# Kernel tuning notes

Measured on AMD Instinct MI355X. Metric: run time of the kernel, lower is better.

Reference implementation:

```python
import jax, jax.numpy as jnp
import numpy as np

N_ELEC = 62      # electrodes per graph (fixed by RGNN/SEED)
BATCH = 4096     # number of graphs
IN_CH = 5
HID = 32
N_CLS = 3
K = 2            # SGConv propagation steps (num_layers)


def setup_inputs() -> dict:
    key = jax.random.key(0)
    k1, k2, k3, k4 = jax.random.split(key, 4)
    n_tril = N_ELEC * (N_ELEC + 1) // 2  # 1953 learned lower-tri weights
    x = jax.random.normal(k1, (BATCH * N_ELEC, IN_CH), jnp.float32)
    adj_tril = jax.random.uniform(k2, (n_tril,), jnp.float32)
    lin_w = jax.random.normal(k3, (HID, IN_CH), jnp.float32) * 0.3
    lin_b = jnp.zeros((HID,), jnp.float32)
    fc_w = jax.random.normal(k4, (N_CLS, HID), jnp.float32) * 0.2
    fc_b = jnp.zeros((N_CLS,), jnp.float32)
    # Dense per-graph edge list matching adj.reshape(-1).repeat(B):
    # edge e = b*3844 + i*62 + j has source row=b*62+i, target col=b*62+j.
    i = np.arange(N_ELEC, dtype=np.int32)
    src = np.repeat(i, N_ELEC)              # [3844]
    dst = np.tile(i, N_ELEC)                # [3844]
    off = (np.arange(BATCH, dtype=np.int32) * N_ELEC)[:, None]
    row = (src[None, :] + off).reshape(-1)  # [B*3844]
    col = (dst[None, :] + off).reshape(-1)
    edge_index = jnp.asarray(np.stack([row, col]))  # int32 [2, E]
    batch_idx = jnp.asarray(np.repeat(np.arange(BATCH, dtype=np.int32), N_ELEC))
    return dict(x=x, adj_tril=adj_tril, lin_w=lin_w, lin_b=lin_b,
                fc_w=fc_w, fc_b=fc_b, edge_index=edge_index, batch_idx=batch_idx)


def reference(x, adj_tril, lin_w, lin_b, fc_w, fc_b, edge_index, batch_idx):
    # Rebuild symmetric dense adjacency from learned lower-triangular params.
    xs, ys = np.tril_indices(N_ELEC)  # static indices
    A = jnp.zeros((N_ELEC, N_ELEC), x.dtype).at[xs, ys].set(adj_tril)
    A = A + A.T - jnp.diag(jnp.diag(A))
    w = jnp.tile(A.reshape(-1), BATCH)        # edge weights [E]
    row, col = edge_index[0], edge_index[1]
    n_nodes = BATCH * N_ELEC
    # Symmetric GCN norm: D^-1/2 A D^-1/2 over the edge list (self-loops
    # already present in the dense graph, so add_remaining_self_loops is a
    # pure edge reorder here).
    deg = jax.ops.segment_sum(jnp.abs(w), row, num_segments=n_nodes)
    safe_deg = jnp.where(deg > 0, deg, 1.0)
    dinv = jnp.where(deg > 0, jax.lax.rsqrt(safe_deg), 0.0)
    norm = dinv[row] * w * dinv[col]          # [E]
    # K rounds of gather-scale-scatter propagation (SGConv).
    h = x
    for _ in range(K):
        h = jax.ops.segment_sum(norm[:, None] * h[row], col, num_segments=n_nodes)
    h = jax.nn.relu(h @ lin_w.T + lin_b)       # SGConv linear + relu
    pooled = jax.ops.segment_sum(h, batch_idx, num_segments=BATCH)  # global_add_pool
    # dropout is identity in eval mode
    return pooled @ fc_w.T + fc_b              # [B, num_classes]
```

## Files before the change

### kernel.cpp

```cpp
#include <hip/hip_runtime.h>

#define NE 62
#define IC 5
#define NTRIL 1953
#define SA 68
#define MTOT 3844

__global__ __launch_bounds__(256) void build_M(const float* __restrict__ adj_tril,
                                               float* __restrict__ Mg) {
    __shared__ float A[NE * SA];
    __shared__ float dinv[NE];
    int tid = threadIdx.x;
    for (int t = tid; t < NTRIL; t += 256) {
        float v = adj_tril[t];
        float r = sqrtf((float)(8 * t + 1));
        int i = (int)((r - 1.0f) * 0.5f);
        while ((i + 1) * (i + 2) / 2 <= t) ++i;
        while (i * (i + 1) / 2 > t) --i;
        int j = t - i * (i + 1) / 2;
        A[i * SA + j] = v;
        A[j * SA + i] = v;
    }
    __syncthreads();
    if (tid < NE) {
        float s = 0.f;
        for (int k = 0; k < NE; ++k) s += fabsf(A[tid * SA + k]);
        dinv[tid] = (s > 0.f) ? rsqrtf(s) : 0.f;
    }
    __syncthreads();
    for (int g = tid; g < NE * NE; g += 256) {
        int i = g / NE, j = g % NE;
        A[i * SA + j] *= dinv[i] * dinv[j];
    }
    __syncthreads();
    int g = blockIdx.x * 256 + tid;
    if (g < NE * NE) {
        int r = g / NE, cidx = g % NE;
        const float4* ra = (const float4*)(A + r * SA);
        const float4* rb = (const float4*)(A + cidx * SA);
        float acc = 0.f;
#pragma unroll
        for (int c = 0; c < 15; ++c) {
            float4 a = ra[c], b = rb[c];
            acc += a.x * b.x + a.y * b.y + a.z * b.z + a.w * b.w;
        }
        acc += A[r * SA + 60] * A[cidx * SA + 60] + A[r * SA + 61] * A[cidx * SA + 61];
        int addr = (cidx < 60) ? ((cidx >> 2) * 248 + r * 4 + (cidx & 3))
                               : (3720 + r * 2 + (cidx - 60));
        Mg[addr] = acc;
    }
}

__global__ __launch_bounds__(256) void forward_k(const float* __restrict__ x,
        const float* __restrict__ lin_w, const float* __restrict__ lin_b,
        const float* __restrict__ fc_w, const float* __restrict__ fc_b,
        const float* __restrict__ Mg, float* __restrict__ out) {
    __shared__ float Mlds[MTOT];
    __shared__ float Xs[4 * 312];
    __shared__ float Ys[4][NE * 12];
    int tid = threadIdx.x;
    {
        const float4* src = (const float4*)Mg;
        float4* dst = (float4*)Mlds;
        for (int t = tid; t < MTOT / 4; t += 256) dst[t] = src[t];
        const float2* xsrc = (const float2*)(x + (size_t)blockIdx.x * (4 * 310));
        for (int t = tid; t < 620; t += 256) {
            int w = t / 155, o = t - w * 155;
            *(float2*)&Xs[w * 312 + o * 2] = xsrc[t];
        }
    }
    int wid = tid >> 6;
    int lane = tid & 63;
    int b = blockIdx.x * 4 + wid;
    int c = lane & 31;
    float w0 = lin_w[c * 5 + 0], w1 = lin_w[c * 5 + 1], w2 = lin_w[c * 5 + 2],
          w3 = lin_w[c * 5 + 3], w4 = lin_w[c * 5 + 4];
    float lb = lin_b[c];
    float f0 = fc_w[c], f1 = fc_w[32 + c], f2 = fc_w[64 + c];
    __syncthreads();
    int j = lane;
    if (j < NE) {
        const float* xb = Xs + wid * 312;
        float y0 = 0, y1 = 0, y2 = 0, y3 = 0, y4 = 0;
#pragma unroll
        for (int ch = 0; ch < 15; ++ch) {
            float4 m = *(const float4*)(Mlds + ch * 248 + j * 4);
            const float4* xi = (const float4*)(xb + ch * 20);
            float4 xa = xi[0], xv = xi[1], xc = xi[2], xd = xi[3], xe = xi[4];
            y0 += m.x * xa.x; y1 += m.x * xa.y; y2 += m.x * xa.z; y3 += m.x * xa.w; y4 += m.x * xv.x;
            y0 += m.y * xv.y; y1 += m.y * xv.z; y2 += m.y * xv.w; y3 += m.y * xc.x; y4 += m.y * xc.y;
            y0 += m.z * xc.z; y1 += m.z * xc.w; y2 += m.z * xd.x; y3 += m.z * xd.y; y4 += m.z * xd.z;
            y0 += m.w * xd.w; y1 += m.w * xe.x; y2 += m.w * xe.y; y3 += m.w * xe.z; y4 += m.w * xe.w;
        }
        float2 mt = *(const float2*)(Mlds + 3720 + j * 2);
        const float* xt = xb + 300;
        y0 += mt.x * xt[0] + mt.y * xt[5];
        y1 += mt.x * xt[1] + mt.y * xt[6];
        y2 += mt.x * xt[2] + mt.y * xt[7];
        y3 += mt.x * xt[3] + mt.y * xt[8];
        y4 += mt.x * xt[4] + mt.y * xt[9];
        float* yr = &Ys[wid][j * 12];
        *(float4*)yr = make_float4(y0, y1, y2, y3);
        yr[4] = y4;
    }
    __syncthreads();
    int half = lane >> 5;
    float acc = 0.f;
    int jbeg = half * 31;
    for (int t = 0; t < 31; ++t) {
        const float* yr = &Ys[wid][(jbeg + t) * 12];
        float4 yv = *(const float4*)yr;
        float d = yv.x * w0 + yv.y * w1 + yv.z * w2 + yv.w * w3 + yr[4] * w4 + lb;
        acc += fmaxf(d, 0.f);
    }
    acc += __shfl_xor(acc, 32, 64);
    float p0 = acc * f0, p1 = acc * f1, p2 = acc * f2;
#pragma unroll
    for (int m = 16; m >= 1; m >>= 1) {
        p0 += __shfl_xor(p0, m, 64);
        p1 += __shfl_xor(p1, m, 64);
        p2 += __shfl_xor(p2, m, 64);
    }
    if (lane == 0) {
        out[b * 3 + 0] = p0 + fc_b[0];
        out[b * 3 + 1] = p1 + fc_b[1];
        out[b * 3 + 2] = p2 + fc_b[2];
    }
}

extern "C" void kernel_launch(void* const* d_in, const int* in_sizes, int n_in,
                              void* d_out, int out_size, void* d_ws, size_t ws_size,
                              hipStream_t stream) {
    const float* x        = (const float*)d_in[0];
    const float* adj_tril = (const float*)d_in[1];
    const float* lin_w    = (const float*)d_in[2];
    const float* lin_b    = (const float*)d_in[3];
    const float* fc_w     = (const float*)d_in[4];
    const float* fc_b     = (const float*)d_in[5];
    float* out = (float*)d_out;
    float* Mg  = (float*)d_ws;

    build_M<<<16, 256, 0, stream>>>(adj_tril, Mg);
    forward_k<<<1024, 256, 0, stream>>>(x, lin_w, lin_b, fc_w, fc_b, Mg, out);
}
```

Measured before the change: 184.3 us.

## Fuse adjacency build into forward kernel and propagate twice per graph

Drops the separate kernel that precomputed the squared normalized adjacency M = (D^-1/2 A D^-1/2)^2 into workspace. Each block now gathers A directly from the lower-triangular parameters into LDS and computes the degree normalization itself. It then runs the two propagation steps per graph, folding the D^-1/2 scaling into the inputs and outputs instead of using a normalized matrix. This removes a launch and the serial dependency on the small setup kernel. In exchange, every block repeats the adjacency gather and degree reduction and does two 62x62 matvec passes instead of one, and it relies on wave-synchronous LDS visibility without barriers.

```diff
diff --git a/kernel.cpp b/kernel.cpp
--- a/kernel.cpp
+++ b/kernel.cpp
@@ -1,90 +1,74 @@
 #include <hip/hip_runtime.h>
 
 #define NE 62
-#define IC 5
 #define NTRIL 1953
-#define SA 68
-#define MTOT 3844
+#define ATOT 3844
 
-__global__ __launch_bounds__(256) void build_M(const float* __restrict__ adj_tril,
-                                               float* __restrict__ Mg) {
-    __shared__ float A[NE * SA];
-    __shared__ float dinv[NE];
-    int tid = threadIdx.x;
-    for (int t = tid; t < NTRIL; t += 256) {
-        float v = adj_tril[t];
-        float r = sqrtf((float)(8 * t + 1));
-        int i = (int)((r - 1.0f) * 0.5f);
-        while ((i + 1) * (i + 2) / 2 <= t) ++i;
-        while (i * (i + 1) / 2 > t) --i;
-        int j = t - i * (i + 1) / 2;
-        A[i * SA + j] = v;
-        A[j * SA + i] = v;
-    }
-    __syncthreads();
-    if (tid < NE) {
-        float s = 0.f;
-        for (int k = 0; k < NE; ++k) s += fabsf(A[tid * SA + k]);
-        dinv[tid] = (s > 0.f) ? rsqrtf(s) : 0.f;
-    }
-    __syncthreads();
-    for (int g = tid; g < NE * NE; g += 256) {
-        int i = g / NE, j = g % NE;
-        A[i * SA + j] *= dinv[i] * dinv[j];
-    }
-    __syncthreads();
-    int g = blockIdx.x * 256 + tid;
-    if (g < NE * NE) {
-        int r = g / NE, cidx = g % NE;
-        const float4* ra = (const float4*)(A + r * SA);
-        const float4* rb = (const float4*)(A + cidx * SA);
-        float acc = 0.f;
-#pragma unroll
-        for (int c = 0; c < 15; ++c) {
-            float4 a = ra[c], b = rb[c];
-            acc += a.x * b.x + a.y * b.y + a.z * b.z + a.w * b.w;
-        }
-        acc += A[r * SA + 60] * A[cidx * SA + 60] + A[r * SA + 61] * A[cidx * SA + 61];
-        int addr = (cidx < 60) ? ((cidx >> 2) * 248 + r * 4 + (cidx & 3))
-                               : (3720 + r * 2 + (cidx - 60));
-        Mg[addr] = acc;
-    }
-}
-
-__global__ __launch_bounds__(256) void forward_k(const float* __restrict__ x,
+__global__ __launch_bounds__(256) void fused_fwd(const float* __restrict__ x,
+        const float* __restrict__ adj_tril,
         const float* __restrict__ lin_w, const float* __restrict__ lin_b,
         const float* __restrict__ fc_w, const float* __restrict__ fc_b,
-        const float* __restrict__ Mg, float* __restrict__ out) {
-    __shared__ float Mlds[MTOT];
+        float* __restrict__ out) {
+    __shared__ float Ac[ATOT];
+    __shared__ float dinv[64];
     __shared__ float Xs[4 * 312];
-    __shared__ float Ys[4][NE * 12];
+    __shared__ float Y1s[4][NE * 8];
+    __shared__ float Y2s[4][NE * 12];
     int tid = threadIdx.x;
+    int wid = tid >> 6;
+    int lane = tid & 63;
+    int b = blockIdx.x * 4 + wid;
+
+    int c = lane & 31;
+    float w0 = lin_w[c * 5 + 0], w1 = lin_w[c * 5 + 1], w2 = lin_w[c * 5 + 2],
+          w3 = lin_w[c * 5 + 3], w4 = lin_w[c * 5 + 4];
+    float lb = lin_b[c];
+    float f0 = fc_w[c], f1 = fc_w[32 + c], f2 = fc_w[64 + c];
+
     {
-        const float4* src = (const float4*)Mg;
-        float4* dst = (float4*)Mlds;
-        for (int t = tid; t < MTOT / 4; t += 256) dst[t] = src[t];
-        const float2* xsrc = (const float2*)(x + (size_t)blockIdx.x * (4 * 310));
+        const float2* xsrc = (const float2*)(x + (size_t)blockIdx.x * 1240);
         for (int t = tid; t < 620; t += 256) {
             int w = t / 155, o = t - w * 155;
             *(float2*)&Xs[w * 312 + o * 2] = xsrc[t];
         }
     }
-    int wid = tid >> 6;
-    int lane = tid & 63;
-    int b = blockIdx.x * 4 + wid;
-    int c = lane & 31;
-    float w0 = lin_w[c * 5 + 0], w1 = lin_w[c * 5 + 1], w2 = lin_w[c * 5 + 2],
-          w3 = lin_w[c * 5 + 3], w4 = lin_w[c * 5 + 4];
-    float lb = lin_b[c];
-    float f0 = fc_w[c], f1 = fc_w[32 + c], f2 = fc_w[64 + c];
+    for (int addr = tid; addr < ATOT; addr += 256) {
+        int i, j;
+        if (addr < 3720) {
+            int ch = addr / 248, rem = addr - ch * 248;
+            j = rem >> 2;
+            i = ch * 4 + (rem & 3);
+        } else {
+            int rem = addr - 3720;
+            j = rem >> 1;
+            i = 60 + (rem & 1);
+        }
+        int a = j > i ? j : i, s = j + i - a;
+        Ac[addr] = adj_tril[a * (a + 1) / 2 + s];
+    }
     __syncthreads();
-    int j = lane;
-    if (j < NE) {
-        const float* xb = Xs + wid * 312;
+    if (tid < NE) {
+        float s = 0.f;
+#pragma unroll
+        for (int ch = 0; ch < 15; ++ch) {
+            float4 a = *(const float4*)(Ac + ch * 248 + tid * 4);
+            s += fabsf(a.x) + fabsf(a.y) + fabsf(a.z) + fabsf(a.w);
+        }
+        s += fabsf(Ac[3720 + tid * 2]) + fabsf(Ac[3721 + tid * 2]);
+        dinv[tid] = (s > 0.f) ? rsqrtf(s) : 0.f;
+    }
+    __syncthreads();
+    float* xb = Xs + wid * 312;
+    if (lane < NE) {
+        float dv = dinv[lane];
+        float* xr = xb + lane * 5;
+        xr[0] *= dv; xr[1] *= dv; xr[2] *= dv; xr[3] *= dv; xr[4] *= dv;
+    }
+    if (lane < NE) {
         float y0 = 0, y1 = 0, y2 = 0, y3 = 0, y4 = 0;
 #pragma unroll
         for (int ch = 0; ch < 15; ++ch) {
-            float4 m = *(const float4*)(Mlds + ch * 248 + j * 4);
+            float4 m = *(const float4*)(Ac + ch * 248 + lane * 4);
             const float4* xi = (const float4*)(xb + ch * 20);
             float4 xa = xi[0], xv = xi[1], xc = xi[2], xd = xi[3], xe = xi[4];
             y0 += m.x * xa.x; y1 += m.x * xa.y; y2 += m.x * xa.z; y3 += m.x * xa.w; y4 += m.x * xv.x;
@@ -92,23 +76,52 @@
             y0 += m.z * xc.z; y1 += m.z * xc.w; y2 += m.z * xd.x; y3 += m.z * xd.y; y4 += m.z * xd.z;
             y0 += m.w * xd.w; y1 += m.w * xe.x; y2 += m.w * xe.y; y3 += m.w * xe.z; y4 += m.w * xe.w;
         }
-        float2 mt = *(const float2*)(Mlds + 3720 + j * 2);
+        float2 mt = *(const float2*)(Ac + 3720 + lane * 2);
         const float* xt = xb + 300;
         y0 += mt.x * xt[0] + mt.y * xt[5];
         y1 += mt.x * xt[1] + mt.y * xt[6];
         y2 += mt.x * xt[2] + mt.y * xt[7];
         y3 += mt.x * xt[3] + mt.y * xt[8];
         y4 += mt.x * xt[4] + mt.y * xt[9];
-        float* yr = &Ys[wid][j * 12];
-        *(float4*)yr = make_float4(y0, y1, y2, y3);
-        yr[4] = y4;
+        float dv = dinv[lane], dv2 = dv * dv;
+        float* yr = &Y1s[wid][lane * 8];
+        *(float4*)yr = make_float4(y0 * dv2, y1 * dv2, y2 * dv2, y3 * dv2);
+        yr[4] = y4 * dv2;
     }
-    __syncthreads();
+    if (lane < NE) {
+        const float* yb = Y1s[wid];
+        float y0 = 0, y1 = 0, y2 = 0, y3 = 0, y4 = 0;
+#pragma unroll
+        for (int ch = 0; ch < 15; ++ch) {
+            float4 m = *(const float4*)(Ac + ch * 248 + lane * 4);
+            const float* r0 = yb + (4 * ch) * 8;
+            float4 a0 = *(const float4*)(r0);      float e0 = r0[4];
+            float4 a1 = *(const float4*)(r0 + 8);  float e1 = r0[12];
+            float4 a2 = *(const float4*)(r0 + 16); float e2 = r0[20];
+            float4 a3 = *(const float4*)(r0 + 24); float e3 = r0[28];
+            y0 += m.x * a0.x; y1 += m.x * a0.y; y2 += m.x * a0.z; y3 += m.x * a0.w; y4 += m.x * e0;
+            y0 += m.y * a1.x; y1 += m.y * a1.y; y2 += m.y * a1.z; y3 += m.y * a1.w; y4 += m.y * e1;
+            y0 += m.z * a2.x; y1 += m.z * a2.y; y2 += m.z * a2.z; y3 += m.z * a2.w; y4 += m.z * e2;
+            y0 += m.w * a3.x; y1 += m.w * a3.y; y2 += m.w * a3.z; y3 += m.w * a3.w; y4 += m.w * e3;
+        }
+        float2 mt = *(const float2*)(Ac + 3720 + lane * 2);
+        const float* r60 = yb + 60 * 8;
+        const float* r61 = yb + 61 * 8;
+        y0 += mt.x * r60[0] + mt.y * r61[0];
+        y1 += mt.x * r60[1] + mt.y * r61[1];
+        y2 += mt.x * r60[2] + mt.y * r61[2];
+        y3 += mt.x * r60[3] + mt.y * r61[3];
+        y4 += mt.x * r60[4] + mt.y * r61[4];
+        float dv = dinv[lane];
+        float* yr = &Y2s[wid][lane * 12];
+        *(float4*)yr = make_float4(y0 * dv, y1 * dv, y2 * dv, y3 * dv);
+        yr[4] = y4 * dv;
+    }
     int half = lane >> 5;
     float acc = 0.f;
     int jbeg = half * 31;
     for (int t = 0; t < 31; ++t) {
-        const float* yr = &Ys[wid][(jbeg + t) * 12];
+        const float* yr = &Y2s[wid][(jbeg + t) * 12];
         float4 yv = *(const float4*)yr;
         float d = yv.x * w0 + yv.y * w1 + yv.z * w2 + yv.w * w3 + yr[4] * w4 + lb;
         acc += fmaxf(d, 0.f);
@@ -138,8 +151,6 @@
     const float* fc_w     = (const float*)d_in[4];
     const float* fc_b     = (const float*)d_in[5];
     float* out = (float*)d_out;
-    float* Mg  = (float*)d_ws;
 
-    build_M<<<16, 256, 0, stream>>>(adj_tril, Mg);
-    forward_k<<<1024, 256, 0, stream>>>(x, lin_w, lin_b, fc_w, fc_b, Mg, out);
+    fused_fwd<<<1024, 256, 0, stream>>>(x, adj_tril, lin_w, lin_b, fc_w, fc_b, out);
 }
```

Measured after the change: 191.0 us. +3.6%, slower.
